# Optimization experiments

Measured on AMD Instinct MI355X. Metric: run time of the kernel, lower is better.

Reference implementation:

```python
import jax, jax.numpy as jnp
import numpy as np

B, W, L = 32768, 5, 20            # batch, words per example, max chars per word
WV, CV = 50000, 100               # word vocab, char vocab
CE, OC, K = 32, 30, 3             # char embed dim, conv out channels (=window_size), kernel
WE, HID, TAGS = 50, 100, 36       # word embed dim, fc1 hidden, output tags


def setup_inputs() -> dict:
    key = jax.random.key(0)
    ks = jax.random.split(key, 8)
    inp = jax.random.randint(ks[0], (B, W, 1 + L), 0, 100, dtype=jnp.int32)
    embedding_matrix = jax.random.normal(ks[1], (WV, WE), jnp.float32).at[0].set(0.0)  # padding_idx=0, frozen
    char_emb = jax.random.normal(ks[2], (CV, CE), jnp.float32).at[0].set(0.0)          # padding_idx=0
    conv_w = jax.random.normal(ks[3], (OC, CE, K), jnp.float32) * 0.1
    conv_b = jnp.zeros((OC,), jnp.float32)
    fc1_w = jax.random.normal(ks[4], (HID, (WE + OC) * W), jnp.float32) * 0.05
    fc1_b = jnp.zeros((HID,), jnp.float32)
    out_w = jax.random.normal(ks[5], (TAGS, HID), jnp.float32) * 0.1
    out_b = jnp.zeros((TAGS,), jnp.float32)
    return dict(input=inp, embedding_matrix=embedding_matrix, char_emb=char_emb,
                conv_w=conv_w, conv_b=conv_b, fc1_w=fc1_w, fc1_b=fc1_b,
                out_w=out_w, out_b=out_b)


def reference(input, embedding_matrix, char_emb, conv_w, conv_b, fc1_w, fc1_b, out_w, out_b):
    b = input.shape[0]
    word_ids = input[:, :, 0]                 # [B, W]
    char_ids = input[:, :, 1:]                # [B, W, L]
    we = embedding_matrix[word_ids]           # [B, W, 50]
    ce = char_emb[char_ids]                   # [B, W, L, CE]
    # conv1d over char axis, batched over all B*W words at once
    x = ce.reshape(b * W, L, CE).transpose(0, 2, 1)        # [B*W, CE, L]
    conv = jax.lax.conv_general_dilated(
        x, conv_w, window_strides=(1,), padding='VALID',
        dimension_numbers=('NCH', 'OIH', 'NCH')) + conv_b[None, :, None]  # [B*W, OC, L-2]
    pooled = conv.max(axis=2).reshape(b, W, OC)            # max pool over time
    feats = jnp.concatenate([we, pooled], axis=-1).reshape(b, -1)  # [B, (50+OC)*W]
    h = jnp.tanh(feats @ fc1_w.T + fc1_b)     # dropout is a no-op at inference
    return h @ out_w.T + out_b                # [B, 36]
```

## Files before the change

### kernel.cpp

```cpp
#include <hip/hip_runtime.h>

#define B_TOT 32768
#define OC 30
#define HID 100
#define TAGS 36

#define WS_TH  0
#define WS_FC1 6000
#define WS_OUT 29296
#define WS_F   40960

typedef __attribute__((ext_vector_type(8))) _Float16 half8;
typedef __attribute__((ext_vector_type(2))) _Float16 h2v;
typedef __attribute__((ext_vector_type(4))) float f32x4;

__device__ inline half8 ash8(uint4 u) {
    union { uint4 a; half8 b; } v; v.a = u; return v.b;
}
__device__ inline unsigned int h2u(h2v h) {
    union { h2v a; unsigned int b; } v; v.a = h; return v.b;
}
__device__ inline h2v u2h(unsigned int u) {
    union { unsigned int a; h2v b; } v; v.a = u; return v.b;
}
__device__ inline unsigned int pk_f16(float a, float b) {
    h2v h; h.x = (_Float16)a; h.y = (_Float16)b; return h2u(h);
}

__global__ void prep(const float* __restrict__ conv_w,
                     const float* __restrict__ char_emb,
                     const float* __restrict__ fc1_w,
                     const float* __restrict__ out_w,
                     unsigned int* __restrict__ ws) {
    int idx = blockIdx.x * 256 + threadIdx.x;
    if (idx < 6000) {
        int rd = idx % 20, row = idx / 20;
        int c = row % 100, k = row / 100;
        float v[2];
        #pragma unroll
        for (int e = 0; e < 2; ++e) {
            int oc = rd * 2 + e;
            float s = 0.f;
            if (oc < OC) {
                for (int ce = 0; ce < 32; ++ce)
                    s += char_emb[c * 32 + ce] * conv_w[(oc * 32 + ce) * 3 + k];
            }
            v[e] = s;
        }
        ws[WS_TH + idx] = pk_f16(v[0], v[1]);
    } else if (idx < 6000 + 23296) {
        int t = idx - 6000;
        int dw = t & 3, lane = (t >> 2) & 63, chunk = t >> 8;
        int ks = chunk % 13, nt = chunk / 13;
        int j = nt * 16 + (lane & 15);
        int k = ks * 32 + (lane >> 4) * 8 + dw * 2;
        float a = (j < HID && k     < 400) ? fc1_w[j * 400 + k]     : 0.f;
        float b = (j < HID && k + 1 < 400) ? fc1_w[j * 400 + k + 1] : 0.f;
        ws[WS_FC1 + t] = pk_f16(a, b);
    } else if (idx < 29296 + 3072) {
        int t = idx - 29296;
        int dw = t & 3, lane = (t >> 2) & 63, chunk = t >> 8;
        int ks = chunk % 4, nt = chunk / 4;
        int j = nt * 16 + (lane & 15);
        int k = ks * 32 + (lane >> 4) * 8 + dw * 2;
        float a = (j < TAGS && k     < HID) ? out_w[j * 100 + k]     : 0.f;
        float b = (j < TAGS && k + 1 < HID) ? out_w[j * 100 + k + 1] : 0.f;
        ws[WS_OUT + t] = pk_f16(a, b);
    }
}

__global__ __launch_bounds__(256)
void feat(const int*   __restrict__ input,
          const float* __restrict__ emb,
          const float* __restrict__ conv_b,
          unsigned int* __restrict__ ws)
{
    __shared__ unsigned int Ths[6000];

    const int tid   = threadIdx.x;
    const int item0 = blockIdx.x * 16;
    unsigned int* Fg = ws + WS_F;

    for (int idx = tid; idx < 6000; idx += 256) Ths[idx] = ws[WS_TH + idx];
    __syncthreads();

    if (tid < 128) Fg[(item0 + (tid >> 3)) * 208 + 200 + (tid & 7)] = 0;

    for (int idx = tid; idx < 2000; idx += 256) {
        int ph = idx % 25;
        int w  = (idx / 25) % 5;
        int i  = idx / 125;
        int wid = input[(item0 + i) * 105 + w * 21];
        float2 e = *(const float2*)&emb[wid * 50 + ph * 2];
        Fg[(item0 + i) * 208 + w * 40 + ph] = pk_f16(e.x, e.y);
    }

    {
        const int q4  = tid & 3;
        const int oc0 = q4 * 8;
        h2v bias[4];
        #pragma unroll
        for (int d = 0; d < 4; ++d) {
            int a = oc0 + 2 * d, b = a + 1;
            bias[d].x = (_Float16)(a < OC ? conv_b[a] : 0.f);
            bias[d].y = (_Float16)(b < OC ? conv_b[b] : 0.f);
        }
        for (int task = tid >> 2; task < 80; task += 64) {
            int i = task / 5, w = task % 5;
            const int* cp = &input[(item0 + i) * 105 + w * 21 + 1];
            int c[20];
            #pragma unroll
            for (int p = 0; p < 20; ++p) c[p] = cp[p];
            h2v m[4];
            #pragma unroll
            for (int d = 0; d < 4; ++d) { m[d].x = (_Float16)(-30000.f); m[d].y = (_Float16)(-30000.f); }
            #pragma unroll 6
            for (int p = 0; p < 18; ++p) {
                uint4 ra = *(const uint4*)&Ths[c[p    ] * 20        + q4 * 4];
                uint4 rb = *(const uint4*)&Ths[c[p + 1] * 20 + 2000 + q4 * 4];
                uint4 rc = *(const uint4*)&Ths[c[p + 2] * 20 + 4000 + q4 * 4];
                unsigned int* pa = (unsigned int*)&ra;
                unsigned int* pb = (unsigned int*)&rb;
                unsigned int* pc = (unsigned int*)&rc;
                #pragma unroll
                for (int d = 0; d < 4; ++d) {
                    h2v s = u2h(pa[d]) + u2h(pb[d]) + u2h(pc[d]);
                    m[d] = __builtin_elementwise_max(m[d], s);
                }
            }
            int base = (item0 + i) * 208 + w * 40 + 25 + q4 * 4;
            Fg[base]     = h2u(m[0] + bias[0]);
            Fg[base + 1] = h2u(m[1] + bias[1]);
            Fg[base + 2] = h2u(m[2] + bias[2]);
            if (q4 < 3) Fg[base + 3] = h2u(m[3] + bias[3]);
        }
    }
}

__global__ __launch_bounds__(256)
void gemm(const float* __restrict__ fc1_b,
          const float* __restrict__ out_b,
          const unsigned int* __restrict__ ws,
          float*       __restrict__ out)
{
    __shared__ unsigned int Hh[4][16 * 68];

    const int tid  = threadIdx.x;
    const int wv   = tid >> 6;
    const int lane = tid & 63;
    const int ln15 = lane & 15;
    const int quad = lane >> 4;
    const int item0 = blockIdx.x * 64 + wv * 16;
    unsigned int* Hw = &Hh[wv][0];
    const unsigned int* Fg = ws + WS_F;

    f32x4 acc[7];
    #pragma unroll
    for (int t = 0; t < 7; ++t) acc[t] = f32x4{0, 0, 0, 0};
    {
        const uint4* wp = (const uint4*)(ws + WS_FC1);
        const unsigned int* arow = Fg + (item0 + ln15) * 208 + quad * 4;
        for (int ks = 0; ks < 13; ++ks) {
            half8 a = ash8(*(const uint4*)(arow + ks * 16));
            #pragma unroll
            for (int t = 0; t < 7; ++t) {
                uint4 bv = wp[(t * 13 + ks) * 64 + lane];
                acc[t] = __builtin_amdgcn_mfma_f32_16x16x32_f16(a, ash8(bv), acc[t], 0, 0, 0);
            }
        }
    }

    {
        for (int t2 = lane; t2 < 224; t2 += 64) {
            int i = t2 / 14, d = t2 % 14;
            Hw[i * 68 + 50 + d] = 0;
        }
        unsigned short* Hs = (unsigned short*)Hw;
        #pragma unroll
        for (int t = 0; t < 7; ++t) {
            int j = t * 16 + ln15;
            if (j < HID) {
                float bj = fc1_b[j];
                #pragma unroll
                for (int r = 0; r < 4; ++r) {
                    int it = quad * 4 + r;
                    float hv = tanhf(acc[t][r] + bj);
                    _Float16 h = (_Float16)hv;
                    Hs[it * 136 + j] = *reinterpret_cast<unsigned short*>(&h);
                }
            }
        }
    }

    {
        f32x4 oacc[3];
        #pragma unroll
        for (int t = 0; t < 3; ++t) oacc[t] = f32x4{0, 0, 0, 0};
        const uint4* wpo = (const uint4*)(ws + WS_OUT);
        const int aoff = ln15 * 68 + quad * 4;
        #pragma unroll
        for (int ks = 0; ks < 4; ++ks) {
            half8 a = ash8(*(const uint4*)&Hw[aoff + ks * 16]);
            #pragma unroll
            for (int t = 0; t < 3; ++t) {
                uint4 bv = wpo[(t * 4 + ks) * 64 + lane];
                oacc[t] = __builtin_amdgcn_mfma_f32_16x16x32_f16(a, ash8(bv), oacc[t], 0, 0, 0);
            }
        }
        #pragma unroll
        for (int t = 0; t < 3; ++t) {
            int o = t * 16 + ln15;
            if (o < TAGS) {
                float bo = out_b[o];
                #pragma unroll
                for (int r = 0; r < 4; ++r) {
                    int it = item0 + quad * 4 + r;
                    out[it * TAGS + o] = oacc[t][r] + bo;
                }
            }
        }
    }
}

extern "C" void kernel_launch(void* const* d_in, const int* in_sizes, int n_in,
                              void* d_out, int out_size, void* d_ws, size_t ws_size,
                              hipStream_t stream) {
    const int*   input  = (const int*)  d_in[0];
    const float* emb    = (const float*)d_in[1];
    const float* char_e = (const float*)d_in[2];
    const float* conv_w = (const float*)d_in[3];
    const float* conv_b = (const float*)d_in[4];
    const float* fc1_w  = (const float*)d_in[5];
    const float* fc1_b  = (const float*)d_in[6];
    const float* out_w  = (const float*)d_in[7];
    const float* out_b  = (const float*)d_in[8];
    unsigned int* ws = (unsigned int*)d_ws;

    prep<<<127, 256, 0, stream>>>(conv_w, char_e, fc1_w, out_w, ws);
    feat<<<B_TOT / 16, 256, 0, stream>>>(input, emb, conv_b, ws);
    gemm<<<B_TOT / 64, 256, 0, stream>>>(fc1_b, out_b, ws, (float*)d_out);
}
```

Before: 129.4 us.

## Enlarge feat blocks and split gemm N-tiles across two waves per item tile

The feature kernel now processes 32 items per 512-thread block, so each copy of the 24KB char-conv table into shared memory serves twice as many items. The gemm kernel is restructured so two waves share one 16-item tile: one wave computes 4 fc1 N-tiles and the other 3, both write tanh outputs into a shared H buffer, then after a barrier they split the output N-tiles 2/1. This cuts per-wave accumulator registers and raises the number of blocks, at the cost of a block barrier and each wave reloading the same A rows.

```diff
diff --git a/kernel.cpp b/kernel.cpp
--- a/kernel.cpp
+++ b/kernel.cpp
@@ -69,7 +69,7 @@
     }
 }
 
-__global__ __launch_bounds__(256)
+__global__ __launch_bounds__(512)
 void feat(const int*   __restrict__ input,
           const float* __restrict__ emb,
           const float* __restrict__ conv_b,
@@ -78,15 +78,15 @@
     __shared__ unsigned int Ths[6000];
 
     const int tid   = threadIdx.x;
-    const int item0 = blockIdx.x * 16;
+    const int item0 = blockIdx.x * 32;
     unsigned int* Fg = ws + WS_F;
 
-    for (int idx = tid; idx < 6000; idx += 256) Ths[idx] = ws[WS_TH + idx];
+    for (int idx = tid; idx < 6000; idx += 512) Ths[idx] = ws[WS_TH + idx];
     __syncthreads();
 
-    if (tid < 128) Fg[(item0 + (tid >> 3)) * 208 + 200 + (tid & 7)] = 0;
-
-    for (int idx = tid; idx < 2000; idx += 256) {
+    if (tid < 256) Fg[(item0 + (tid >> 3)) * 208 + 200 + (tid & 7)] = 0;
+
+    for (int idx = tid; idx < 4000; idx += 512) {
         int ph = idx % 25;
         int w  = (idx / 25) % 5;
         int i  = idx / 125;
@@ -105,7 +105,7 @@
             bias[d].x = (_Float16)(a < OC ? conv_b[a] : 0.f);
             bias[d].y = (_Float16)(b < OC ? conv_b[b] : 0.f);
         }
-        for (int task = tid >> 2; task < 80; task += 64) {
+        for (int task = tid >> 2; task < 160; task += 128) {
             int i = task / 5, w = task % 5;
             const int* cp = &input[(item0 + i) * 105 + w * 21 + 1];
             int c[20];
@@ -137,85 +137,99 @@
     }
 }
 
-__global__ __launch_bounds__(256)
+__global__ __launch_bounds__(128)
 void gemm(const float* __restrict__ fc1_b,
           const float* __restrict__ out_b,
           const unsigned int* __restrict__ ws,
           float*       __restrict__ out)
 {
-    __shared__ unsigned int Hh[4][16 * 68];
+    __shared__ unsigned int Hh[16 * 68];
 
     const int tid  = threadIdx.x;
     const int wv   = tid >> 6;
     const int lane = tid & 63;
     const int ln15 = lane & 15;
     const int quad = lane >> 4;
-    const int item0 = blockIdx.x * 64 + wv * 16;
-    unsigned int* Hw = &Hh[wv][0];
+    const int item0 = blockIdx.x * 16;
     const unsigned int* Fg = ws + WS_F;
 
-    f32x4 acc[7];
+    const int t0 = wv ? 4 : 0;
+    const int tn = wv ? 3 : 4;
+    f32x4 acc[4];
     #pragma unroll
-    for (int t = 0; t < 7; ++t) acc[t] = f32x4{0, 0, 0, 0};
+    for (int t = 0; t < 4; ++t) acc[t] = f32x4{0, 0, 0, 0};
     {
         const uint4* wp = (const uint4*)(ws + WS_FC1);
         const unsigned int* arow = Fg + (item0 + ln15) * 208 + quad * 4;
         for (int ks = 0; ks < 13; ++ks) {
             half8 a = ash8(*(const uint4*)(arow + ks * 16));
             #pragma unroll
-            for (int t = 0; t < 7; ++t) {
-                uint4 bv = wp[(t * 13 + ks) * 64 + lane];
-                acc[t] = __builtin_amdgcn_mfma_f32_16x16x32_f16(a, ash8(bv), acc[t], 0, 0, 0);
-            }
-        }
-    }
-
-    {
+            for (int t = 0; t < 4; ++t) {
+                if (t < tn) {
+                    uint4 bv = wp[((t0 + t) * 13 + ks) * 64 + lane];
+                    acc[t] = __builtin_amdgcn_mfma_f32_16x16x32_f16(a, ash8(bv), acc[t], 0, 0, 0);
+                }
+            }
+        }
+    }
+
+    if (wv == 1) {
         for (int t2 = lane; t2 < 224; t2 += 64) {
             int i = t2 / 14, d = t2 % 14;
-            Hw[i * 68 + 50 + d] = 0;
-        }
-        unsigned short* Hs = (unsigned short*)Hw;
-        #pragma unroll
-        for (int t = 0; t < 7; ++t) {
-            int j = t * 16 + ln15;
-            if (j < HID) {
-                float bj = fc1_b[j];
-                #pragma unroll
-                for (int r = 0; r < 4; ++r) {
-                    int it = quad * 4 + r;
-                    float hv = tanhf(acc[t][r] + bj);
-                    _Float16 h = (_Float16)hv;
-                    Hs[it * 136 + j] = *reinterpret_cast<unsigned short*>(&h);
-                }
-            }
-        }
-    }
-
-    {
-        f32x4 oacc[3];
-        #pragma unroll
-        for (int t = 0; t < 3; ++t) oacc[t] = f32x4{0, 0, 0, 0};
+            Hh[i * 68 + 50 + d] = 0;
+        }
+    }
+    {
+        unsigned short* Hs = (unsigned short*)Hh;
+        #pragma unroll
+        for (int t = 0; t < 4; ++t) {
+            if (t < tn) {
+                int j = (t0 + t) * 16 + ln15;
+                if (j < HID) {
+                    float bj = fc1_b[j];
+                    #pragma unroll
+                    for (int r = 0; r < 4; ++r) {
+                        int it = quad * 4 + r;
+                        float hv = tanhf(acc[t][r] + bj);
+                        _Float16 h = (_Float16)hv;
+                        Hs[it * 136 + j] = *reinterpret_cast<unsigned short*>(&h);
+                    }
+                }
+            }
+        }
+    }
+    __syncthreads();
+
+    {
+        const int ot0 = wv ? 2 : 0;
+        const int otn = wv ? 1 : 2;
+        f32x4 oacc[2];
+        #pragma unroll
+        for (int t = 0; t < 2; ++t) oacc[t] = f32x4{0, 0, 0, 0};
         const uint4* wpo = (const uint4*)(ws + WS_OUT);
         const int aoff = ln15 * 68 + quad * 4;
         #pragma unroll
         for (int ks = 0; ks < 4; ++ks) {
-            half8 a = ash8(*(const uint4*)&Hw[aoff + ks * 16]);
-            #pragma unroll
-            for (int t = 0; t < 3; ++t) {
-                uint4 bv = wpo[(t * 4 + ks) * 64 + lane];
-                oacc[t] = __builtin_amdgcn_mfma_f32_16x16x32_f16(a, ash8(bv), oacc[t], 0, 0, 0);
-            }
-        }
-        #pragma unroll
-        for (int t = 0; t < 3; ++t) {
-            int o = t * 16 + ln15;
-            if (o < TAGS) {
-                float bo = out_b[o];
-                #pragma unroll
-                for (int r = 0; r < 4; ++r) {
-                    int it = item0 + quad * 4 + r;
-                    out[it * TAGS + o] = oacc[t][r] + bo;
+            half8 a = ash8(*(const uint4*)&Hh[aoff + ks * 16]);
+            #pragma unroll
+            for (int t = 0; t < 2; ++t) {
+                if (t < otn) {
+                    uint4 bv = wpo[((ot0 + t) * 4 + ks) * 64 + lane];
+                    oacc[t] = __builtin_amdgcn_mfma_f32_16x16x32_f16(a, ash8(bv), oacc[t], 0, 0, 0);
+                }
+            }
+        }
+        #pragma unroll
+        for (int t = 0; t < 2; ++t) {
+            if (t < otn) {
+                int o = (ot0 + t) * 16 + ln15;
+                if (o < TAGS) {
+                    float bo = out_b[o];
+                    #pragma unroll
+                    for (int r = 0; r < 4; ++r) {
+                        int it = item0 + quad * 4 + r;
+                        out[it * TAGS + o] = oacc[t][r] + bo;
+                    }
                 }
             }
         }
@@ -237,6 +251,6 @@
     unsigned int* ws = (unsigned int*)d_ws;
 
     prep<<<127, 256, 0, stream>>>(conv_w, char_e, fc1_w, out_w, ws);
-    feat<<<B_TOT / 16, 256, 0, stream>>>(input, emb, conv_b, ws);
-    gemm<<<B_TOT / 64, 256, 0, stream>>>(fc1_b, out_b, ws, (float*)d_out);
-}
+    feat<<<B_TOT / 32, 512, 0, stream>>>(input, emb, conv_b, ws);
+    gemm<<<B_TOT / 16, 128, 0, stream>>>(fc1_b, out_b, ws, (float*)d_out);
+}
```

Measured after the change: 131.7 us. No clear change (+1.8%).
